# Performance work log

Measured on AMD Instinct MI355X. Metric: run time of the kernel, lower is better.

Reference implementation:

```python
import jax, jax.numpy as jnp
import numpy as np

NUM_HEADS = 16


def setup_inputs() -> dict:
    key = jax.random.key(0)
    ks = jax.random.split(key, 5)
    b, s, d = 2, 2048, 1024
    std = (2.0 / (d + d)) ** 0.5
    x = jax.random.normal(ks[0], (b, s, d), dtype=jnp.float32)
    Wq = jax.random.normal(ks[1], (d, d), dtype=jnp.float32) * std
    Wk = jax.random.normal(ks[2], (d, d), dtype=jnp.float32) * std
    Wv = jax.random.normal(ks[3], (d, d), dtype=jnp.float32) * std
    Wo = jax.random.normal(ks[4], (d, d), dtype=jnp.float32) * std
    return {"x": x, "Wq": Wq, "Wk": Wk, "Wv": Wv, "Wo": Wo}


def reference(x, Wq, Wk, Wv, Wo):
    b, s, d = x.shape
    h = NUM_HEADS
    dk = d // h
    # projections: bias-free x @ W (W is [in, out])
    def split_heads(t):
        return t.reshape(b, s, h, dk).transpose(0, 2, 1, 3)  # b h s dk
    q = split_heads(x @ Wq)
    k = split_heads(x @ Wk)
    v = split_heads(x @ Wv)
    scale = 1.0 / jnp.sqrt(jnp.asarray(dk, dtype=x.dtype))
    scores = jnp.einsum('bhqd,bhkd->bhqk', q, k) * scale  # b h s s
    causal = jnp.tril(jnp.ones((s, s), dtype=bool))
    scores = jnp.where(causal, scores, -jnp.inf)
    probs = jax.nn.softmax(scores, axis=-1)
    out = jnp.einsum('bhqk,bhkd->bhqd', probs, v)
    out = out.transpose(0, 2, 1, 3).reshape(b, s, d)  # b s (h dk)
    return out @ Wo
```

## Files before the change

kernel.cpp:

```cpp
#include <hip/hip_runtime.h>

typedef unsigned short u16;
typedef unsigned int   u32;

using bf16x8 = __attribute__((ext_vector_type(8))) __bf16;
using f32x4  = __attribute__((ext_vector_type(4))) float;
using s16x4  = __attribute__((ext_vector_type(4))) short;

#define NH    16
#define DKH   64
#define SEQ   2048
#define BAT   2
#define DMOD  1024

#define QSCALE 0.18033688011112042f

__device__ __forceinline__ u16 f2bf(float f) {
  union { float f; u32 u; } v; v.f = f;
  u32 r = v.u + 0x7fffu + ((v.u >> 16) & 1u);
  return (u16)(r >> 16);
}

__device__ __forceinline__ u32 pack2bf(float a, float b) {
  union { float f; u32 u; } x, y; x.f = a; y.f = b;
  u32 ua = x.u + 0x7fffu + ((x.u >> 16) & 1u);
  u32 ub = y.u + 0x7fffu + ((y.u >> 16) & 1u);
  return __builtin_amdgcn_perm(ub, ua, 0x07060302u);
}

#if __has_builtin(__builtin_amdgcn_exp2f)
#define EXP2(x) __builtin_amdgcn_exp2f(x)
#else
#define EXP2(x) exp2f(x)
#endif

#if __has_builtin(__builtin_amdgcn_mfma_f32_16x16x16bf16_1k)
__device__ __forceinline__ f32x4 mfma16(s16x4 a, s16x4 b, f32x4 c) {
  return __builtin_amdgcn_mfma_f32_16x16x16bf16_1k(a, b, c, 0, 0, 0);
}
#else
__device__ __forceinline__ f32x4 mfma16(s16x4 a, s16x4 b, f32x4 c) {
  f32x4 d;
  asm volatile("v_mfma_f32_16x16x16_bf16 %0, %1, %2, %3\n\ts_nop 7\n\ts_nop 7"
               : "=v"(d) : "v"(a), "v"(b), "v"(c));
  return d;
}
#endif

__global__ __launch_bounds__(256) void transpose_all(const float* __restrict__ Wq,
                                                     const float* __restrict__ Wk,
                                                     const float* __restrict__ Wv,
                                                     const float* __restrict__ Wo,
                                                     u16* __restrict__ Wt) {
  __shared__ u16 t[32][33];
  const float* W = blockIdx.z == 0 ? Wq : blockIdx.z == 1 ? Wk : blockIdx.z == 2 ? Wv : Wo;
  u16* o = Wt + (size_t)blockIdx.z * DMOD * DMOD;
  int bx = blockIdx.x * 32, by = blockIdx.y * 32;
  int x = threadIdx.x, y = threadIdx.y;
  #pragma unroll
  for (int i = 0; i < 32; i += 8)
    t[y + i][x] = f2bf(W[(size_t)(by + y + i) * DMOD + bx + x]);
  __syncthreads();
  #pragma unroll
  for (int i = 0; i < 32; i += 8)
    o[(size_t)(bx + y + i) * DMOD + by + x] = t[x][y + i];
}

__global__ __launch_bounds__(256) void convert_x(const float* __restrict__ x,
                                                 u16* __restrict__ xb) {
  size_t i = ((size_t)blockIdx.x * 256 + threadIdx.x) * 8;
  float4 f0 = *(const float4*)(x + i);
  float4 f1 = *(const float4*)(x + i + 4);
  uint4 o;
  o.x = pack2bf(f0.x, f0.y); o.y = pack2bf(f0.z, f0.w);
  o.z = pack2bf(f1.x, f1.y); o.w = pack2bf(f1.z, f1.w);
  *(uint4*)(xb + i) = o;
}

__global__ __launch_bounds__(256, 3) void gemm_qkv(const u16* __restrict__ A,
                                                   const u16* __restrict__ Bt,
                                                   u16* __restrict__ Qo,
                                                   u16* __restrict__ Ko,
                                                   u16* __restrict__ Vo) {
  __shared__ __align__(16) u16 As[128 * 40];
  __shared__ __align__(16) u16 Bs[128 * 40];
  const int tid  = threadIdx.x;
  const int lane = tid & 63, wv = tid >> 6;
  const int wm   = wv >> 1, wn = wv & 1;
  const int lrow = lane & 15, quad = lane >> 4;
  const int tileM = blockIdx.x * 128, tileN = blockIdx.y * 128;
  const int r0 = tid >> 2, c0 = (tid & 3) * 8;
  const int r1 = r0 + 64;

  const f32x4 fz = {0.f, 0.f, 0.f, 0.f};
  f32x4 acc[4][4];
  #pragma unroll
  for (int i = 0; i < 4; ++i)
    #pragma unroll
    for (int j = 0; j < 4; ++j) acc[i][j] = fz;

  uint4 a0 = *(const uint4*)(&A [(size_t)(tileM + r0) * DMOD + c0]);
  uint4 a1 = *(const uint4*)(&A [(size_t)(tileM + r1) * DMOD + c0]);
  uint4 b0 = *(const uint4*)(&Bt[(size_t)(tileN + r0) * DMOD + c0]);
  uint4 b1 = *(const uint4*)(&Bt[(size_t)(tileN + r1) * DMOD + c0]);

  for (int kt = 0; kt < DMOD; kt += 32) {
    __syncthreads();
    *(uint4*)(&As[r0 * 40 + c0]) = a0;
    *(uint4*)(&As[r1 * 40 + c0]) = a1;
    *(uint4*)(&Bs[r0 * 40 + c0]) = b0;
    *(uint4*)(&Bs[r1 * 40 + c0]) = b1;
    if (kt + 32 < DMOD) {
      a0 = *(const uint4*)(&A [(size_t)(tileM + r0) * DMOD + kt + 32 + c0]);
      a1 = *(const uint4*)(&A [(size_t)(tileM + r1) * DMOD + kt + 32 + c0]);
      b0 = *(const uint4*)(&Bt[(size_t)(tileN + r0) * DMOD + kt + 32 + c0]);
      b1 = *(const uint4*)(&Bt[(size_t)(tileN + r1) * DMOD + kt + 32 + c0]);
    }
    __syncthreads();
    bf16x8 af[4], bfr[4];
    #pragma unroll
    for (int mt = 0; mt < 4; ++mt)
      af[mt] = *(const bf16x8*)(&As[(wm * 64 + mt * 16 + lrow) * 40 + quad * 8]);
    #pragma unroll
    for (int nt = 0; nt < 4; ++nt)
      bfr[nt] = *(const bf16x8*)(&Bs[(wn * 64 + nt * 16 + lrow) * 40 + quad * 8]);
    #pragma unroll
    for (int mt = 0; mt < 4; ++mt)
      #pragma unroll
      for (int nt = 0; nt < 4; ++nt)
        acc[mt][nt] = __builtin_amdgcn_mfma_f32_16x16x32_bf16(af[mt], bfr[nt],
                                                              acc[mt][nt], 0, 0, 0);
  }

  #pragma unroll
  for (int mt = 0; mt < 4; ++mt) {
    #pragma unroll
    for (int nt = 0; nt < 4; ++nt) {
      int gm0 = tileM + wm * 64 + mt * 16 + quad * 4;
      int gn  = tileN + wn * 64 + nt * 16 + lrow;
      int which = gn >> 10, col = gn & 1023;
      int bb = gm0 >> 11, srw0 = gm0 & (SEQ - 1);
      int hh = col >> 6, dki = col & (DKH - 1);
      size_t bhi = (size_t)(bb * NH + hh);
      if (which == 0) {
        #pragma unroll
        for (int r = 0; r < 4; ++r)
          Qo[(bhi * SEQ + srw0 + r) * DKH + dki] = f2bf(acc[mt][nt][r] * QSCALE);
      } else if (which == 1) {
        #pragma unroll
        for (int r = 0; r < 4; ++r)
          Ko[(bhi * SEQ + srw0 + r) * DKH + dki] = f2bf(acc[mt][nt][r]);
      } else {
        uint2 pk;
        pk.x = pack2bf(acc[mt][nt][0], acc[mt][nt][1]);
        pk.y = pack2bf(acc[mt][nt][2], acc[mt][nt][3]);
        *(uint2*)(&Vo[(((bhi * (SEQ / 4)) + (srw0 >> 2)) * DKH + dki) * 4]) = pk;
      }
    }
  }
}

__global__ __launch_bounds__(256, 3) void gemm_out(const u16* __restrict__ A,
                                                   const u16* __restrict__ Bt,
                                                   float* __restrict__ Co) {
  __shared__ __align__(16) u16 As[128 * 40];
  __shared__ __align__(16) u16 Bs[64 * 40];
  const int tid  = threadIdx.x;
  const int lane = tid & 63, wv = tid >> 6;
  const int wm   = wv & 1, wn = wv >> 1;
  const int lrow = lane & 15, quad = lane >> 4;
  const int tileM = blockIdx.x * 128, tileN = blockIdx.y * 64;
  const int r0 = tid >> 2, c0 = (tid & 3) * 8;
  const int r1 = r0 + 64;

  const f32x4 fz = {0.f, 0.f, 0.f, 0.f};
  f32x4 acc[4][2];
  #pragma unroll
  for (int i = 0; i < 4; ++i) { acc[i][0] = fz; acc[i][1] = fz; }

  uint4 a0 = *(const uint4*)(&A [(size_t)(tileM + r0) * DMOD + c0]);
  uint4 a1 = *(const uint4*)(&A [(size_t)(tileM + r1) * DMOD + c0]);
  uint4 b0 = *(const uint4*)(&Bt[(size_t)(tileN + (r0 & 63)) * DMOD + c0]);

  for (int kt = 0; kt < DMOD; kt += 32) {
    __syncthreads();
    *(uint4*)(&As[r0 * 40 + c0]) = a0;
    *(uint4*)(&As[r1 * 40 + c0]) = a1;
    if (r0 < 64) *(uint4*)(&Bs[r0 * 40 + c0]) = b0;
    if (kt + 32 < DMOD) {
      a0 = *(const uint4*)(&A [(size_t)(tileM + r0) * DMOD + kt + 32 + c0]);
      a1 = *(const uint4*)(&A [(size_t)(tileM + r1) * DMOD + kt + 32 + c0]);
      b0 = *(const uint4*)(&Bt[(size_t)(tileN + (r0 & 63)) * DMOD + kt + 32 + c0]);
    }
    __syncthreads();
    bf16x8 af[4], bfr[2];
    #pragma unroll
    for (int mt = 0; mt < 4; ++mt)
      af[mt] = *(const bf16x8*)(&As[(wm * 64 + mt * 16 + lrow) * 40 + quad * 8]);
    #pragma unroll
    for (int nt = 0; nt < 2; ++nt)
      bfr[nt] = *(const bf16x8*)(&Bs[(wn * 32 + nt * 16 + lrow) * 40 + quad * 8]);
    #pragma unroll
    for (int mt = 0; mt < 4; ++mt)
      #pragma unroll
      for (int nt = 0; nt < 2; ++nt)
        acc[mt][nt] = __builtin_amdgcn_mfma_f32_16x16x32_bf16(af[mt], bfr[nt],
                                                              acc[mt][nt], 0, 0, 0);
  }

  #pragma unroll
  for (int mt = 0; mt < 4; ++mt)
    #pragma unroll
    for (int nt = 0; nt < 2; ++nt)
      #pragma unroll
      for (int r = 0; r < 4; ++r) {
        int gm = tileM + wm * 64 + mt * 16 + quad * 4 + r;
        int gn = tileN + wn * 32 + nt * 16 + lrow;
        Co[(size_t)gm * DMOD + gn] = acc[mt][nt][r];
      }
}

#define KP 72
#define VP 132

__global__ __launch_bounds__(256, 2) void attn_k(const u16* __restrict__ Q,
                                                 const u16* __restrict__ Kg,
                                                 const u16* __restrict__ Vg,
                                                 u16* __restrict__ Og) {
  __shared__ __align__(16) u16 KsA[128 * KP];
  __shared__ __align__(16) u16 VsA[64 * VP];
  __shared__ __align__(16) u16 KsB[128 * KP];
  __shared__ __align__(16) u16 VsB[64 * VP];

  const int tid  = threadIdx.x;
  const int lane = tid & 63, w = tid >> 6;
  const int lrow = lane & 15, quad = lane >> 4;
  const int bh = blockIdx.x;
  const int t  = blockIdx.y;
  const int qt = (t < 8) ? t : 23 - t;
  const int b = bh >> 4, h = bh & 15;

  const u16* Qbh = Q  + (size_t)bh * SEQ * DKH;
  const u16* Kbh = Kg + (size_t)bh * SEQ * DKH;
  const u16* Vbh = Vg + (size_t)bh * SEQ * DKH;

  const int jmax = qt;

  bf16x8 bq[2][2];
  #pragma unroll
  for (int s = 0; s < 2; ++s)
    #pragma unroll
    for (int kk = 0; kk < 2; ++kk)
      bq[s][kk] = *(const bf16x8*)(&Qbh[(size_t)(qt * 128 + (2 * w + s) * 16 + lrow) * DKH
                                        + kk * 32 + quad * 8]);

  uint4 kreg[4], vreg[4];
  #pragma unroll
  for (int k = 0; k < 4; ++k) {
    int ci = k * 256 + tid;
    kreg[k] = *(const uint4*)(&Kbh[(size_t)(ci >> 3) * DKH + (ci & 7) * 8]);
    vreg[k] = *(const uint4*)(&Vbh[(size_t)(ci >> 5) * 256 + (ci & 31) * 8]);
  }

  const f32x4 fz = {0.f, 0.f, 0.f, 0.f};
  f32x4 oacc[2][4];
  #pragma unroll
  for (int s = 0; s < 2; ++s)
    #pragma unroll
    for (int d = 0; d < 4; ++d) oacc[s][d] = fz;
  float lsum[2] = {0.f, 0.f};

  int cur = 0;
  for (int j = 0; j <= jmax; ++j) {
    u16* Ks = cur ? KsB : KsA;
    u16* Vs = cur ? VsB : VsA;

    #pragma unroll
    for (int k = 0; k < 4; ++k) {
      int ci = k * 256 + tid;
      *(uint4*)(&Ks[(ci >> 3) * KP + (ci & 7) * 8]) = kreg[k];
      int sq = ci >> 5, dkp = ci & 31;
      union { uint4 q; uint2 d[2]; } vv; vv.q = vreg[k];
      *(uint2*)(&Vs[(2 * dkp)     * VP + 4 * sq]) = vv.d[0];
      *(uint2*)(&Vs[(2 * dkp + 1) * VP + 4 * sq]) = vv.d[1];
    }

    if (j < jmax) {
      const int jn = j + 1;
      #pragma unroll
      for (int k = 0; k < 4; ++k) {
        int ci = k * 256 + tid;
        kreg[k] = *(const uint4*)(&Kbh[(size_t)(jn * 128 + (ci >> 3)) * DKH + (ci & 7) * 8]);
        vreg[k] = *(const uint4*)(&Vbh[(size_t)(jn * 32 + (ci >> 5)) * 256 + (ci & 31) * 8]);
      }
    }

    __syncthreads();

    if (j < jmax) {
      f32x4 sacc[2][8];
      #pragma unroll
      for (int s = 0; s < 2; ++s)
        #pragma unroll
        for (int m = 0; m < 8; ++m) sacc[s][m] = fz;
      #pragma unroll
      for (int kk = 0; kk < 2; ++kk)
        #pragma unroll
        for (int m = 0; m < 8; ++m) {
          bf16x8 ak = *(const bf16x8*)(&Ks[(m * 16 + lrow) * KP + kk * 32 + quad * 8]);
          sacc[0][m] = __builtin_amdgcn_mfma_f32_16x16x32_bf16(ak, bq[0][kk], sacc[0][m], 0, 0, 0);
          sacc[1][m] = __builtin_amdgcn_mfma_f32_16x16x32_bf16(ak, bq[1][kk], sacc[1][m], 0, 0, 0);
        }
      #pragma unroll
      for (int m = 0; m < 8; ++m) {
        float p00 = EXP2(sacc[0][m][0]), p01 = EXP2(sacc[0][m][1]);
        float p02 = EXP2(sacc[0][m][2]), p03 = EXP2(sacc[0][m][3]);
        float p10 = EXP2(sacc[1][m][0]), p11 = EXP2(sacc[1][m][1]);
        float p12 = EXP2(sacc[1][m][2]), p13 = EXP2(sacc[1][m][3]);
        lsum[0] += (p00 + p01) + (p02 + p03);
        lsum[1] += (p10 + p11) + (p12 + p13);
        union { u32 u[2]; s16x4 v; } pk0, pk1;
        pk0.u[0] = pack2bf(p00, p01); pk0.u[1] = pack2bf(p02, p03);
        pk1.u[0] = pack2bf(p10, p11); pk1.u[1] = pack2bf(p12, p13);
        #pragma unroll
        for (int d = 0; d < 4; ++d) {
          s16x4 av = *(const s16x4*)(&Vs[(d * 16 + lrow) * VP + m * 16 + quad * 4]);
          oacc[0][d] = mfma16(av, pk0.v, oacc[0][d]);
          oacc[1][d] = mfma16(av, pk1.v, oacc[1][d]);
        }
      }
    } else {
      #pragma unroll
      for (int s = 0; s < 2; ++s) {
        const int ws = 2 * w + s;
        for (int m = 0; m < ws; ++m) {
          f32x4 sv = fz;
          #pragma unroll
          for (int kk = 0; kk < 2; ++kk) {
            bf16x8 ak = *(const bf16x8*)(&Ks[(m * 16 + lrow) * KP + kk * 32 + quad * 8]);
            sv = __builtin_amdgcn_mfma_f32_16x16x32_bf16(ak, bq[s][kk], sv, 0, 0, 0);
          }
          float p0 = EXP2(sv[0]), p1 = EXP2(sv[1]), p2 = EXP2(sv[2]), p3 = EXP2(sv[3]);
          lsum[s] += (p0 + p1) + (p2 + p3);
          union { u32 u[2]; s16x4 v; } pk;
          pk.u[0] = pack2bf(p0, p1); pk.u[1] = pack2bf(p2, p3);
          #pragma unroll
          for (int d = 0; d < 4; ++d) {
            s16x4 av = *(const s16x4*)(&Vs[(d * 16 + lrow) * VP + m * 16 + quad * 4]);
            oacc[s][d] = mfma16(av, pk.v, oacc[s][d]);
          }
        }
        {
          f32x4 sv = fz;
          #pragma unroll
          for (int kk = 0; kk < 2; ++kk) {
            bf16x8 ak = *(const bf16x8*)(&Ks[(ws * 16 + lrow) * KP + kk * 32 + quad * 8]);
            sv = __builtin_amdgcn_mfma_f32_16x16x32_bf16(ak, bq[s][kk], sv, 0, 0, 0);
          }
          float p[4];
          #pragma unroll
          for (int r = 0; r < 4; ++r)
            p[r] = (quad * 4 + r > lrow) ? 0.f : EXP2(sv[r]);
          lsum[s] += (p[0] + p[1]) + (p[2] + p[3]);
          union { u32 u[2]; s16x4 v; } pk;
          pk.u[0] = pack2bf(p[0], p[1]); pk.u[1] = pack2bf(p[2], p[3]);
          #pragma unroll
          for (int d = 0; d < 4; ++d) {
            s16x4 av = *(const s16x4*)(&Vs[(d * 16 + lrow) * VP + ws * 16 + quad * 4]);
            oacc[s][d] = mfma16(av, pk.v, oacc[s][d]);
          }
        }
      }
    }
    cur ^= 1;
  }

  #pragma unroll
  for (int s = 0; s < 2; ++s) {
    float ls = lsum[s];
    ls += __shfl_xor(ls, 16, 64);
    ls += __shfl_xor(ls, 32, 64);
    float inv = 1.f / ls;
    int qrow = qt * 128 + (2 * w + s) * 16 + lrow;
    #pragma unroll
    for (int d = 0; d < 4; ++d) {
      uint2 pkk;
      pkk.x = pack2bf(oacc[s][d][0] * inv, oacc[s][d][1] * inv);
      pkk.y = pack2bf(oacc[s][d][2] * inv, oacc[s][d][3] * inv);
      *(uint2*)(&Og[(size_t)(b * SEQ + qrow) * DMOD + h * DKH + d * 16 + quad * 4]) = pkk;
    }
  }
}

extern "C" void kernel_launch(void* const* d_in, const int* in_sizes, int n_in,
                              void* d_out, int out_size, void* d_ws, size_t ws_size,
                              hipStream_t stream) {
  const float* x  = (const float*)d_in[0];
  const float* Wq = (const float*)d_in[1];
  const float* Wk = (const float*)d_in[2];
  const float* Wv = (const float*)d_in[3];
  const float* Wo = (const float*)d_in[4];

  u16* ws = (u16*)d_ws;
  const size_t WSZ = (size_t)DMOD * DMOD;
  const size_t TSZ = (size_t)BAT * NH * SEQ * DKH;
  u16* Wt  = ws;
  u16* Wto = Wt + 3 * WSZ;
  u16* xb  = Wt + 4 * WSZ;
  u16* Qb  = xb + TSZ;
  u16* Kb  = Qb + TSZ;
  u16* Vb  = Kb + TSZ;
  u16* Ob  = xb;

  transpose_all<<<dim3(32, 32, 4), dim3(32, 8), 0, stream>>>(Wq, Wk, Wv, Wo, Wt);
  convert_x<<<dim3(2048), 256, 0, stream>>>(x, xb);

  gemm_qkv<<<dim3(32, 24), 256, 0, stream>>>(xb, Wt, Qb, Kb, Vb);

  attn_k<<<dim3(32, 16), 256, 0, stream>>>(Qb, Kb, Vb, Ob);

  gemm_out<<<dim3(32, 16), 256, 0, stream>>>(Ob, Wto, (float*)d_out);
}
```

Measured before the change: 177.9 us.

## Halve attention query tile to 64 rows, single-buffer LDS, stage output through LDS

The attention kernel now uses 128-thread blocks, each handling 64 query rows instead of 128, which doubles the grid to 1024 blocks. K/V shared memory drops from double to single buffering, with a barrier at the top of each iteration. The output tile is written to LDS and then stored to global memory with coalesced 16-byte writes. Bf16 packing now uses a native bf16 conversion helper. The aim is more parallelism and occupancy from smaller blocks and less LDS per block. The cost is more K/V reloads per query row and an extra synchronization per tile.

```diff
diff --git a/kernel.cpp b/kernel.cpp
--- a/kernel.cpp
+++ b/kernel.cpp
@@ -4,6 +4,7 @@
 typedef unsigned int   u32;
 
 using bf16x8 = __attribute__((ext_vector_type(8))) __bf16;
+using bf16x4 = __attribute__((ext_vector_type(4))) __bf16;
 using f32x4  = __attribute__((ext_vector_type(4))) float;
 using s16x4  = __attribute__((ext_vector_type(4))) short;
 
@@ -26,6 +27,12 @@
   u32 ua = x.u + 0x7fffu + ((x.u >> 16) & 1u);
   u32 ub = y.u + 0x7fffu + ((y.u >> 16) & 1u);
   return __builtin_amdgcn_perm(ub, ua, 0x07060302u);
+}
+
+__device__ __forceinline__ s16x4 pk4bf(float a, float b, float c, float d) {
+  union { bf16x4 bv; s16x4 sv; } u;
+  u.bv[0] = (__bf16)a; u.bv[1] = (__bf16)b; u.bv[2] = (__bf16)c; u.bv[3] = (__bf16)d;
+  return u.sv;
 }
 
 #if __has_builtin(__builtin_amdgcn_exp2f)
@@ -222,42 +229,41 @@
 
 #define KP 72
 #define VP 132
-
-__global__ __launch_bounds__(256, 2) void attn_k(const u16* __restrict__ Q,
+#define OP 68
+
+__global__ __launch_bounds__(128, 2) void attn_k(const u16* __restrict__ Q,
                                                  const u16* __restrict__ Kg,
                                                  const u16* __restrict__ Vg,
                                                  u16* __restrict__ Og) {
-  __shared__ __align__(16) u16 KsA[128 * KP];
-  __shared__ __align__(16) u16 VsA[64 * VP];
-  __shared__ __align__(16) u16 KsB[128 * KP];
-  __shared__ __align__(16) u16 VsB[64 * VP];
+  __shared__ __align__(16) u16 Ks[128 * KP];
+  __shared__ __align__(16) u16 Vs[64 * VP];
 
   const int tid  = threadIdx.x;
   const int lane = tid & 63, w = tid >> 6;
   const int lrow = lane & 15, quad = lane >> 4;
   const int bh = blockIdx.x;
   const int t  = blockIdx.y;
-  const int qt = (t < 8) ? t : 23 - t;
+  const int qb = (t < 16) ? t : 47 - t;
   const int b = bh >> 4, h = bh & 15;
+  const int jmax = qb >> 1;
+  const int qoff = qb & 1;
 
   const u16* Qbh = Q  + (size_t)bh * SEQ * DKH;
   const u16* Kbh = Kg + (size_t)bh * SEQ * DKH;
   const u16* Vbh = Vg + (size_t)bh * SEQ * DKH;
 
-  const int jmax = qt;
-
   bf16x8 bq[2][2];
   #pragma unroll
   for (int s = 0; s < 2; ++s)
     #pragma unroll
     for (int kk = 0; kk < 2; ++kk)
-      bq[s][kk] = *(const bf16x8*)(&Qbh[(size_t)(qt * 128 + (2 * w + s) * 16 + lrow) * DKH
+      bq[s][kk] = *(const bf16x8*)(&Qbh[(size_t)(qb * 64 + (2 * w + s) * 16 + lrow) * DKH
                                         + kk * 32 + quad * 8]);
 
-  uint4 kreg[4], vreg[4];
-  #pragma unroll
-  for (int k = 0; k < 4; ++k) {
-    int ci = k * 256 + tid;
+  uint4 kreg[8], vreg[8];
+  #pragma unroll
+  for (int k = 0; k < 8; ++k) {
+    int ci = k * 128 + tid;
     kreg[k] = *(const uint4*)(&Kbh[(size_t)(ci >> 3) * DKH + (ci & 7) * 8]);
     vreg[k] = *(const uint4*)(&Vbh[(size_t)(ci >> 5) * 256 + (ci & 31) * 8]);
   }
@@ -270,14 +276,12 @@
     for (int d = 0; d < 4; ++d) oacc[s][d] = fz;
   float lsum[2] = {0.f, 0.f};
 
-  int cur = 0;
   for (int j = 0; j <= jmax; ++j) {
-    u16* Ks = cur ? KsB : KsA;
-    u16* Vs = cur ? VsB : VsA;
-
-    #pragma unroll
-    for (int k = 0; k < 4; ++k) {
-      int ci = k * 256 + tid;
+    if (j) __syncthreads();
+
+    #pragma unroll
+    for (int k = 0; k < 8; ++k) {
+      int ci = k * 128 + tid;
       *(uint4*)(&Ks[(ci >> 3) * KP + (ci & 7) * 8]) = kreg[k];
       int sq = ci >> 5, dkp = ci & 31;
       union { uint4 q; uint2 d[2]; } vv; vv.q = vreg[k];
@@ -288,8 +292,8 @@
     if (j < jmax) {
       const int jn = j + 1;
       #pragma unroll
-      for (int k = 0; k < 4; ++k) {
-        int ci = k * 256 + tid;
+      for (int k = 0; k < 8; ++k) {
+        int ci = k * 128 + tid;
         kreg[k] = *(const uint4*)(&Kbh[(size_t)(jn * 128 + (ci >> 3)) * DKH + (ci & 7) * 8]);
         vreg[k] = *(const uint4*)(&Vbh[(size_t)(jn * 32 + (ci >> 5)) * 256 + (ci & 31) * 8]);
       }
@@ -319,21 +323,20 @@
         float p12 = EXP2(sacc[1][m][2]), p13 = EXP2(sacc[1][m][3]);
         lsum[0] += (p00 + p01) + (p02 + p03);
         lsum[1] += (p10 + p11) + (p12 + p13);
-        union { u32 u[2]; s16x4 v; } pk0, pk1;
-        pk0.u[0] = pack2bf(p00, p01); pk0.u[1] = pack2bf(p02, p03);
-        pk1.u[0] = pack2bf(p10, p11); pk1.u[1] = pack2bf(p12, p13);
+        s16x4 pk0 = pk4bf(p00, p01, p02, p03);
+        s16x4 pk1 = pk4bf(p10, p11, p12, p13);
         #pragma unroll
         for (int d = 0; d < 4; ++d) {
           s16x4 av = *(const s16x4*)(&Vs[(d * 16 + lrow) * VP + m * 16 + quad * 4]);
-          oacc[0][d] = mfma16(av, pk0.v, oacc[0][d]);
-          oacc[1][d] = mfma16(av, pk1.v, oacc[1][d]);
+          oacc[0][d] = mfma16(av, pk0, oacc[0][d]);
+          oacc[1][d] = mfma16(av, pk1, oacc[1][d]);
         }
       }
     } else {
       #pragma unroll
       for (int s = 0; s < 2; ++s) {
-        const int ws = 2 * w + s;
-        for (int m = 0; m < ws; ++m) {
+        const int L = qoff * 4 + 2 * w + s;
+        for (int m = 0; m < L; ++m) {
           f32x4 sv = fz;
           #pragma unroll
           for (int kk = 0; kk < 2; ++kk) {
@@ -342,19 +345,18 @@
           }
           float p0 = EXP2(sv[0]), p1 = EXP2(sv[1]), p2 = EXP2(sv[2]), p3 = EXP2(sv[3]);
           lsum[s] += (p0 + p1) + (p2 + p3);
-          union { u32 u[2]; s16x4 v; } pk;
-          pk.u[0] = pack2bf(p0, p1); pk.u[1] = pack2bf(p2, p3);
+          s16x4 pk = pk4bf(p0, p1, p2, p3);
           #pragma unroll
           for (int d = 0; d < 4; ++d) {
             s16x4 av = *(const s16x4*)(&Vs[(d * 16 + lrow) * VP + m * 16 + quad * 4]);
-            oacc[s][d] = mfma16(av, pk.v, oacc[s][d]);
+            oacc[s][d] = mfma16(av, pk, oacc[s][d]);
           }
         }
         {
           f32x4 sv = fz;
           #pragma unroll
           for (int kk = 0; kk < 2; ++kk) {
-            bf16x8 ak = *(const bf16x8*)(&Ks[(ws * 16 + lrow) * KP + kk * 32 + quad * 8]);
+            bf16x8 ak = *(const bf16x8*)(&Ks[(L * 16 + lrow) * KP + kk * 32 + quad * 8]);
             sv = __builtin_amdgcn_mfma_f32_16x16x32_bf16(ak, bq[s][kk], sv, 0, 0, 0);
           }
           float p[4];
@@ -362,33 +364,46 @@
           for (int r = 0; r < 4; ++r)
             p[r] = (quad * 4 + r > lrow) ? 0.f : EXP2(sv[r]);
           lsum[s] += (p[0] + p[1]) + (p[2] + p[3]);
-          union { u32 u[2]; s16x4 v; } pk;
-          pk.u[0] = pack2bf(p[0], p[1]); pk.u[1] = pack2bf(p[2], p[3]);
+          s16x4 pk = pk4bf(p[0], p[1], p[2], p[3]);
           #pragma unroll
           for (int d = 0; d < 4; ++d) {
-            s16x4 av = *(const s16x4*)(&Vs[(d * 16 + lrow) * VP + ws * 16 + quad * 4]);
-            oacc[s][d] = mfma16(av, pk.v, oacc[s][d]);
+            s16x4 av = *(const s16x4*)(&Vs[(d * 16 + lrow) * VP + L * 16 + quad * 4]);
+            oacc[s][d] = mfma16(av, pk, oacc[s][d]);
           }
         }
       }
     }
-    cur ^= 1;
-  }
-
+  }
+
+  float inv[2];
   #pragma unroll
   for (int s = 0; s < 2; ++s) {
     float ls = lsum[s];
     ls += __shfl_xor(ls, 16, 64);
     ls += __shfl_xor(ls, 32, 64);
-    float inv = 1.f / ls;
-    int qrow = qt * 128 + (2 * w + s) * 16 + lrow;
+    inv[s] = 1.f / ls;
+  }
+
+  __syncthreads();
+  u16* Osr = Ks;
+  #pragma unroll
+  for (int s = 0; s < 2; ++s) {
+    int row = (2 * w + s) * 16 + lrow;
     #pragma unroll
     for (int d = 0; d < 4; ++d) {
       uint2 pkk;
-      pkk.x = pack2bf(oacc[s][d][0] * inv, oacc[s][d][1] * inv);
-      pkk.y = pack2bf(oacc[s][d][2] * inv, oacc[s][d][3] * inv);
-      *(uint2*)(&Og[(size_t)(b * SEQ + qrow) * DMOD + h * DKH + d * 16 + quad * 4]) = pkk;
-    }
+      pkk.x = pack2bf(oacc[s][d][0] * inv[s], oacc[s][d][1] * inv[s]);
+      pkk.y = pack2bf(oacc[s][d][2] * inv[s], oacc[s][d][3] * inv[s]);
+      *(uint2*)(&Osr[row * OP + d * 16 + quad * 4]) = pkk;
+    }
+  }
+  __syncthreads();
+  #pragma unroll
+  for (int k = 0; k < 4; ++k) {
+    int c = k * 128 + tid;
+    int row = c >> 3, ch = c & 7;
+    uint4 v = *(const uint4*)(&Osr[row * OP + ch * 8]);
+    *(uint4*)(&Og[(size_t)(b * SEQ + qb * 64 + row) * DMOD + h * DKH + ch * 8]) = v;
   }
 }
 
@@ -417,7 +432,7 @@
 
   gemm_qkv<<<dim3(32, 24), 256, 0, stream>>>(xb, Wt, Qb, Kb, Vb);
 
-  attn_k<<<dim3(32, 16), 256, 0, stream>>>(Qb, Kb, Vb, Ob);
+  attn_k<<<dim3(32, 32), 128, 0, stream>>>(Qb, Kb, Vb, Ob);
 
   gemm_out<<<dim3(32, 16), 256, 0, stream>>>(Ob, Wto, (float*)d_out);
 }
```

After: 195.1 us. +9.6%, slower.
